# Performance work log

Hardware: AMD Instinct MI355X
Metric: run time of the kernel (lower is better)

The kernel has to match this reference:

```python
import jax, jax.numpy as jnp
import numpy as np

B, T, C, H = 65536, 100, 7, 2  # batch, timesteps, covariates, lstm hidden


def setup_inputs() -> dict:
    key = jax.random.key(0)
    ks = iter(jax.random.split(key, 32))
    def rn(shape, s=0.1):
        return jax.random.normal(next(ks), shape, dtype=jnp.float32) * s
    inp = {"x": jax.random.normal(next(ks), (B, T, C), dtype=jnp.float32)}
    for l, din in ((0, C), (1, 2 * H)):
        for suf in ("", "r"):
            inp[f"w_ih_l{l}{suf}"] = rn((4 * H, din))
            inp[f"w_hh_l{l}{suf}"] = rn((4 * H, H))
            inp[f"b_ih_l{l}{suf}"] = rn((4 * H,))
            inp[f"b_hh_l{l}{suf}"] = rn((4 * H,))
    inp["fc1_w"] = rn((64, 4 * T))
    inp["fc1_b"] = rn((64,))
    inp["fc2_w"] = rn((20, 64))
    inp["fc2_b"] = rn((20,))
    return inp


def _lstm_dir(xw, w_hh, b_hh, reverse):
    # xw: [T, B, 4H] precomputed input projection (x @ W_ih.T + b_ih)
    if reverse:
        xw = xw[::-1]
    h0 = jnp.zeros((xw.shape[1], H), xw.dtype)
    c0 = jnp.zeros((xw.shape[1], H), xw.dtype)

    def step(carry, gx):
        h, c = carry
        g = gx + h @ w_hh.T + b_hh            # [B, 4H]
        i, f, gg, o = jnp.split(g, 4, axis=-1)  # torch gate order i,f,g,o
        c = jax.nn.sigmoid(f) * c + jax.nn.sigmoid(i) * jnp.tanh(gg)
        h = jax.nn.sigmoid(o) * jnp.tanh(c)
        return (h, c), h

    _, hs = jax.lax.scan(step, (h0, c0), xw)
    if reverse:
        hs = hs[::-1]
    return hs  # [T, B, H]


def _bilstm_layer(x_tbf, w_ih_f, w_hh_f, b_ih_f, b_hh_f,
                  w_ih_b, w_hh_b, b_ih_b, b_hh_b):
    xw_f = jnp.einsum('tbc,gc->tbg', x_tbf, w_ih_f) + b_ih_f
    xw_b = jnp.einsum('tbc,gc->tbg', x_tbf, w_ih_b) + b_ih_b
    hf = _lstm_dir(xw_f, w_hh_f, b_hh_f, False)
    hb = _lstm_dir(xw_b, w_hh_b, b_hh_b, True)
    return jnp.concatenate([hf, hb], axis=-1)  # [T, B, 2H]


def reference(x,
              w_ih_l0, w_hh_l0, b_ih_l0, b_hh_l0,
              w_ih_l0r, w_hh_l0r, b_ih_l0r, b_hh_l0r,
              w_ih_l1, w_hh_l1, b_ih_l1, b_hh_l1,
              w_ih_l1r, w_hh_l1r, b_ih_l1r, b_hh_l1r,
              fc1_w, fc1_b, fc2_w, fc2_b):
    xt = jnp.transpose(x.reshape(-1, T, C), (1, 0, 2))  # [T, B, C] time-major
    h1 = _bilstm_layer(xt, w_ih_l0, w_hh_l0, b_ih_l0, b_hh_l0,
                       w_ih_l0r, w_hh_l0r, b_ih_l0r, b_hh_l0r)
    h2 = _bilstm_layer(h1, w_ih_l1, w_hh_l1, b_ih_l1, b_hh_l1,
                       w_ih_l1r, w_hh_l1r, b_ih_l1r, b_hh_l1r)
    out = jnp.transpose(h2, (1, 0, 2)).reshape(-1, 4 * T)  # flatten [B, 4T]
    out = jax.nn.relu(out)                  # relu BEFORE fc1, as in original
    out = jax.nn.relu(out @ fc1_w.T + fc1_b)
    return out @ fc2_w.T + fc2_b            # [B, 20]
```

## Files before the change

kernel.cpp:

```cpp
#include <hip/hip_runtime.h>

#define Bn 65536
#define Tn 100
#define Cn 7

typedef short short8 __attribute__((ext_vector_type(8)));
typedef float float4v __attribute__((ext_vector_type(4)));

__device__ __forceinline__ float fast_rcp(float x) { return __builtin_amdgcn_rcpf(x); }
__device__ __forceinline__ float sig_f(float x) { return fast_rcp(1.f + __expf(-x)); }
__device__ __forceinline__ float tanh_f(float x) { return 1.f - 2.f * fast_rcp(__expf(2.f * x) + 1.f); }
__device__ __forceinline__ unsigned bf16rne(float x) {
    unsigned u = __float_as_uint(x);
    return (u + 0x7fffu + ((u >> 16) & 1u)) >> 16;
}
__device__ __forceinline__ float bf_lo(unsigned u) { return __uint_as_float(u << 16); }
__device__ __forceinline__ float bf_hi(unsigned u) { return __uint_as_float(u & 0xffff0000u); }

typedef const __attribute__((address_space(1))) void* gp_t;
typedef __attribute__((address_space(3))) void* sp_t;
__device__ __forceinline__ void async_copy_dw(const void* g, void* l) {
    __builtin_amdgcn_global_load_lds((gp_t)g, (sp_t)l, 4, 0, 0);
}

__global__ void w2prep_kernel(const float* __restrict__ fc1_w, unsigned short* __restrict__ w2g) {
    int idx = blockIdx.x * 256 + threadIdx.x;
    int w  = idx >> 12;
    int d  = (idx >> 11) & 1;
    int n  = (idx >> 5) & 63;
    int kk = idx & 31;
    int tt = kk >> 1, i = kk & 1;
    int t  = d ? (99 - 10 * w - tt) : (10 * w + tt);
    float v = (kk < 20) ? fc1_w[n * 400 + 4 * t + 2 * d + i] : 0.f;
    w2g[idx] = (unsigned short)bf16rne(v);
}

__global__ __launch_bounds__(256) void l0_kernel(
    const float* __restrict__ x,
    const float* __restrict__ wih_f, const float* __restrict__ whh_f,
    const float* __restrict__ bih_f, const float* __restrict__ bhh_f,
    const float* __restrict__ wih_r, const float* __restrict__ whh_r,
    const float* __restrict__ bih_r, const float* __restrict__ bhh_r,
    unsigned* __restrict__ h1u)
{
    __shared__ float xs[2][2][4480];

    const int tid  = threadIdx.x;
    const int rev  = tid >> 7;
    const int s    = tid & 127;
    const int b    = blockIdx.x * 128 + s;
    const int w    = tid >> 6;
    const int lane = tid & 63;
    const int sdir = w >> 1;
    const int half = w & 1;

    const float* wih = rev ? wih_r : wih_f;
    const float* whh = rev ? whh_r : whh_f;
    const float* bih = rev ? bih_r : bih_f;
    const float* bhh = rev ? bhh_r : bhh_f;

    float wi[56], wh[16], bias[8];
#pragma unroll
    for (int k = 0; k < 56; ++k) wi[k] = wih[k];
#pragma unroll
    for (int k = 0; k < 16; ++k) wh[k] = whh[k];
#pragma unroll
    for (int k = 0; k < 8; ++k) bias[k] = bih[k] + bhh[k];

    const int e  = (lane >= 35) ? 1 : 0;
    const int r0 = lane - 35 * e;
    const int s0 = half * 64 + e;
    const float* xsamp = x + (size_t)(blockIdx.x * 128 + s0) * 700;

    auto stage = [&](int ch, int p) {
        const int off = sdir ? (665 - 35 * ch) : (35 * ch);
        const float* g = xsamp + off + r0;
        float* l = &xs[p][sdir][half * 2240 + lane];
        int r = r0;
#pragma unroll
        for (int i = 0; i < 35; ++i) {
            async_copy_dw(g, l);
            l += 64;
            const int c = (r >= 6) ? 1 : 0;
            g += c ? 1394 : 729;
            r += c ? -6 : 29;
        }
    };

    float h0 = 0.f, h1v = 0.f, c0 = 0.f, c1 = 0.f;

    stage(0, 0);
#pragma unroll 1
    for (int ch = 0; ch < 20; ++ch) {
        if (ch == 0) __builtin_amdgcn_s_waitcnt(0x0F70);
        else         __builtin_amdgcn_s_waitcnt(0x0F75);
        __syncthreads();
        if (ch < 19) stage(ch + 1, (ch + 1) & 1);
        __builtin_amdgcn_sched_barrier(0);

        const int t0 = rev ? (95 - 5 * ch) : (5 * ch);
        const float* xbuf = &xs[ch & 1][rev][0];
#pragma unroll
        for (int tt = 0; tt < 5; ++tt) {
            const int rr = rev ? (4 - tt) : tt;
            const int t  = t0 + rr;
            const float* xrow = xbuf + s * 35 + rr * 7;

            float g[8];
#pragma unroll
            for (int k = 0; k < 8; ++k) g[k] = bias[k];
#pragma unroll
            for (int c = 0; c < 7; ++c) {
                const float xv = xrow[c];
#pragma unroll
                for (int k = 0; k < 8; ++k) g[k] = fmaf(wi[k * 7 + c], xv, g[k]);
            }
#pragma unroll
            for (int k = 0; k < 8; ++k)
                g[k] = fmaf(wh[k * 2], h0, fmaf(wh[k * 2 + 1], h1v, g[k]));

            const float i0 = sig_f(g[0]), i1 = sig_f(g[1]);
            const float f0 = sig_f(g[2]), f1 = sig_f(g[3]);
            const float q0 = tanh_f(g[4]), q1 = tanh_f(g[5]);
            const float o0 = sig_f(g[6]), o1 = sig_f(g[7]);
            c0 = fmaf(f0, c0, i0 * q0);
            c1 = fmaf(f1, c1, i1 * q1);
            h0  = o0 * tanh_f(c0);
            h1v = o1 * tanh_f(c1);

            h1u[((size_t)t * 2 + rev) * Bn + b] = bf16rne(h0) | (bf16rne(h1v) << 16);
        }
    }
}

__global__ __launch_bounds__(256) void l1fc_kernel(
    const unsigned* __restrict__ hin,
    const float* __restrict__ wih_f, const float* __restrict__ whh_f,
    const float* __restrict__ bih_f, const float* __restrict__ bhh_f,
    const float* __restrict__ wih_r, const float* __restrict__ whh_r,
    const float* __restrict__ bih_r, const float* __restrict__ bhh_r,
    const unsigned* __restrict__ w2g,
    const float* __restrict__ fc1_b,
    const float* __restrict__ fc2_w,
    const float* __restrict__ fc2_b,
    float* __restrict__ out)
{
    __shared__ unsigned smem[19456];
    unsigned* a2  = smem;
    unsigned* w2b = smem + 5120;
    unsigned* hst = smem + 9216;

    const int tid  = threadIdx.x;
    const int ww   = tid >> 6;
    const int lane = tid & 63;
    const int d    = ww >> 1;
    const int half = ww & 1;
    const int sm   = half * 64 + lane;
    const int b0   = blockIdx.x * 128;

    const float* wih = d ? wih_r : wih_f;
    const float* whh = d ? whh_r : whh_f;
    const float* bih = d ? bih_r : bih_f;
    const float* bhh = d ? bhh_r : bhh_f;

    float wi[32], wh[16], bias[8];
#pragma unroll
    for (int k = 0; k < 32; ++k) wi[k] = wih[k];
#pragma unroll
    for (int k = 0; k < 16; ++k) wh[k] = whh[k];
#pragma unroll
    for (int k = 0; k < 8; ++k) bias[k] = bih[k] + bhh[k];

    float4v acc[2][4];
#pragma unroll
    for (int mt = 0; mt < 2; ++mt)
#pragma unroll
        for (int nt = 0; nt < 4; ++nt) acc[mt][nt] = (float4v){0.f, 0.f, 0.f, 0.f};

    for (int i = tid; i < 5120; i += 256) a2[i] = 0u;

    auto stage_h = [&](int w, int pb) {
        unsigned* dst = hst + pb * 5120;
        const int Rb = tid >> 7;
        const int s  = tid & 127;
#pragma unroll
        for (int i = 0; i < 20; ++i) {
            const int R  = Rb + 2 * i;
            const int dd = (R >= 20) ? 1 : 0;
            const int r2 = R - 20 * dd;
            const int p  = (r2 >= 10) ? 1 : 0;
            const int j  = r2 - 10 * p;
            const int t  = dd ? (99 - (10 * w + j)) : (10 * w + j);
            async_copy_dw(hin + ((size_t)t * 2 + p) * Bn + b0 + s, dst + R * 128 + s);
        }
    };
    auto stage_w = [&](int w, int pb) {
        const unsigned* src = w2g + w * 2048;
        unsigned* dst = w2b + pb * 2048;
#pragma unroll
        for (int i = 0; i < 8; ++i)
            async_copy_dw(src + i * 256 + tid, dst + i * 256 + tid);
    };

    stage_h(0, 0); stage_w(0, 0);

    float h0 = 0.f, h1v = 0.f, c0 = 0.f, c1 = 0.f;
    const int q = lane >> 4, l16 = lane & 15;

#pragma unroll 1
    for (int w = 0; w < 10; ++w) {
        __builtin_amdgcn_s_waitcnt(0x0F70);
        __syncthreads();
        if (w < 9) { stage_h(w + 1, (w + 1) & 1); stage_w(w + 1, (w + 1) & 1); }

        const unsigned* hb = hst + (w & 1) * 5120 + d * 2560;
#pragma unroll 2
        for (int j = 0; j < 10; ++j) {
            const unsigned uF = hb[j * 128 + sm];
            const unsigned uR = hb[1280 + j * 128 + sm];
            const float aF0 = bf_lo(uF), aF1 = bf_hi(uF);
            const float aR0 = bf_lo(uR), aR1 = bf_hi(uR);

            float g[8];
#pragma unroll
            for (int k = 0; k < 8; ++k) {
                g[k] = bias[k];
                g[k] = fmaf(wi[k * 4 + 0], aF0, g[k]);
                g[k] = fmaf(wi[k * 4 + 1], aF1, g[k]);
                g[k] = fmaf(wi[k * 4 + 2], aR0, g[k]);
                g[k] = fmaf(wi[k * 4 + 3], aR1, g[k]);
                g[k] = fmaf(wh[k * 2], h0, fmaf(wh[k * 2 + 1], h1v, g[k]));
            }
            const float i0 = sig_f(g[0]), i1 = sig_f(g[1]);
            const float f0 = sig_f(g[2]), f1 = sig_f(g[3]);
            const float q0 = tanh_f(g[4]), q1 = tanh_f(g[5]);
            const float o0 = sig_f(g[6]), o1 = sig_f(g[7]);
            c0 = fmaf(f0, c0, i0 * q0);
            c1 = fmaf(f1, c1, i1 * q1);
            h0  = o0 * tanh_f(c0);
            h1v = o1 * tanh_f(c1);

            a2[d * 2560 + sm * 20 + j] = bf16rne(fmaxf(h0, 0.f)) | (bf16rne(fmaxf(h1v, 0.f)) << 16);
        }
        __syncthreads();

        {
            const unsigned* wb = w2b + (w & 1) * 2048;
#pragma unroll
            for (int dd = 0; dd < 2; ++dd) {
                short8 av[2], bv[4];
#pragma unroll
                for (int mt = 0; mt < 2; ++mt)
                    av[mt] = *(const short8*)&a2[dd * 2560 + (ww * 32 + mt * 16 + l16) * 20 + q * 4];
#pragma unroll
                for (int nt = 0; nt < 4; ++nt)
                    bv[nt] = *(const short8*)&wb[dd * 1024 + (nt * 16 + l16) * 16 + q * 4];
#pragma unroll
                for (int mt = 0; mt < 2; ++mt)
#pragma unroll
                    for (int nt = 0; nt < 4; ++nt)
                        acc[mt][nt] = __builtin_amdgcn_mfma_f32_16x16x32_bf16(
                            av[mt], bv[nt], acc[mt][nt], 0, 0, 0);
            }
        }
    }
    __syncthreads();

    {
        float* eb = (float*)smem;
#pragma unroll
        for (int mt = 0; mt < 2; ++mt)
#pragma unroll
            for (int nt = 0; nt < 4; ++nt)
#pragma unroll
                for (int r = 0; r < 4; ++r) {
                    const int sl = ww * 32 + mt * 16 + q * 4 + r;
                    const int cl = nt * 16 + l16;
                    eb[sl * 65 + cl] = acc[mt][nt][r];
                }
    }
    __syncthreads();

    const float* eb = (const float*)smem;
    const int sm2 = tid & 127;
    const int og  = (tid >> 7) * 10;
    float z[64];
#pragma unroll
    for (int k = 0; k < 64; ++k) z[k] = fmaxf(eb[sm2 * 65 + k] + fc1_b[k], 0.f);
    float y[10];
#pragma unroll
    for (int o = 0; o < 10; ++o) {
        float r2 = fc2_b[og + o];
#pragma unroll
        for (int k = 0; k < 64; ++k) r2 = fmaf(fc2_w[(og + o) * 64 + k], z[k], r2);
        y[o] = r2;
    }
    __syncthreads();
    float* ebw = (float*)smem;
#pragma unroll
    for (int o = 0; o < 10; ++o) ebw[sm2 * 20 + og + o] = y[o];
    __syncthreads();
    for (int f = tid; f < 2560; f += 256)
        out[(size_t)blockIdx.x * 2560 + f] = ebw[f];
}

extern "C" void kernel_launch(void* const* d_in, const int* in_sizes, int n_in,
                              void* d_out, int out_size, void* d_ws, size_t ws_size,
                              hipStream_t stream) {
    const float* x = (const float*)d_in[0];
    const float* w_ih_l0  = (const float*)d_in[1];
    const float* w_hh_l0  = (const float*)d_in[2];
    const float* b_ih_l0  = (const float*)d_in[3];
    const float* b_hh_l0  = (const float*)d_in[4];
    const float* w_ih_l0r = (const float*)d_in[5];
    const float* w_hh_l0r = (const float*)d_in[6];
    const float* b_ih_l0r = (const float*)d_in[7];
    const float* b_hh_l0r = (const float*)d_in[8];
    const float* w_ih_l1  = (const float*)d_in[9];
    const float* w_hh_l1  = (const float*)d_in[10];
    const float* b_ih_l1  = (const float*)d_in[11];
    const float* b_hh_l1  = (const float*)d_in[12];
    const float* w_ih_l1r = (const float*)d_in[13];
    const float* w_hh_l1r = (const float*)d_in[14];
    const float* b_ih_l1r = (const float*)d_in[15];
    const float* b_hh_l1r = (const float*)d_in[16];
    const float* fc1_w = (const float*)d_in[17];
    const float* fc1_b = (const float*)d_in[18];
    const float* fc2_w = (const float*)d_in[19];
    const float* fc2_b = (const float*)d_in[20];

    unsigned* h1u = (unsigned*)d_ws;
    unsigned short* w2g = (unsigned short*)((char*)d_ws + (size_t)Tn * 2 * Bn * 4);

    w2prep_kernel<<<160, 256, 0, stream>>>(fc1_w, w2g);
    l0_kernel<<<512, 256, 0, stream>>>(x,
        w_ih_l0, w_hh_l0, b_ih_l0, b_hh_l0,
        w_ih_l0r, w_hh_l0r, b_ih_l0r, b_hh_l0r, h1u);
    l1fc_kernel<<<512, 256, 0, stream>>>(h1u,
        w_ih_l1, w_hh_l1, b_ih_l1, b_hh_l1,
        w_ih_l1r, w_hh_l1r, b_ih_l1r, b_hh_l1r,
        (const unsigned*)w2g, fc1_b, fc2_w, fc2_b, (float*)d_out);
}
```

Measured before the change: 433.5 us.

## Split LSTM hidden units across lane pairs with DPP exchange, double threads

```diff
diff --git a/kernel.cpp b/kernel.cpp
--- a/kernel.cpp
+++ b/kernel.cpp
@@ -16,6 +16,11 @@
 }
 __device__ __forceinline__ float bf_lo(unsigned u) { return __uint_as_float(u << 16); }
 __device__ __forceinline__ float bf_hi(unsigned u) { return __uint_as_float(u & 0xffff0000u); }
+
+__device__ __forceinline__ float dpp_xor1(float x) {
+    return __uint_as_float((unsigned)__builtin_amdgcn_mov_dpp(
+        (int)__float_as_uint(x), 0xB1, 0xF, 0xF, true));
+}
 
 typedef const __attribute__((address_space(1))) void* gp_t;
 typedef __attribute__((address_space(3))) void* sp_t;
@@ -35,7 +40,7 @@
     w2g[idx] = (unsigned short)bf16rne(v);
 }
 
-__global__ __launch_bounds__(256) void l0_kernel(
+__global__ __launch_bounds__(512) void l0_kernel(
     const float* __restrict__ x,
     const float* __restrict__ wih_f, const float* __restrict__ whh_f,
     const float* __restrict__ bih_f, const float* __restrict__ bhh_f,
@@ -46,36 +51,40 @@
     __shared__ float xs[2][2][4480];
 
     const int tid  = threadIdx.x;
-    const int rev  = tid >> 7;
-    const int s    = tid & 127;
+    const int wv   = tid >> 6;
+    const int lane = tid & 63;
+    const int rev  = tid >> 8;
+    const int cid  = tid & 1;
+    const int s    = (tid & 255) >> 1;
     const int b    = blockIdx.x * 128 + s;
-    const int w    = tid >> 6;
-    const int lane = tid & 63;
-    const int sdir = w >> 1;
-    const int half = w & 1;
 
     const float* wih = rev ? wih_r : wih_f;
     const float* whh = rev ? whh_r : whh_f;
     const float* bih = rev ? bih_r : bih_f;
     const float* bhh = rev ? bhh_r : bhh_f;
 
-    float wi[56], wh[16], bias[8];
-#pragma unroll
-    for (int k = 0; k < 56; ++k) wi[k] = wih[k];
-#pragma unroll
-    for (int k = 0; k < 16; ++k) wh[k] = whh[k];
-#pragma unroll
-    for (int k = 0; k < 8; ++k) bias[k] = bih[k] + bhh[k];
-
+    float wi[28], whA[4], whB[4], bias4[4];
+#pragma unroll
+    for (int j = 0; j < 4; ++j) {
+        const int k = cid + 2 * j;
+#pragma unroll
+        for (int c = 0; c < 7; ++c) wi[j * 7 + c] = wih[k * 7 + c];
+        whA[j] = whh[k * 2 + cid];
+        whB[j] = whh[k * 2 + (cid ^ 1)];
+        bias4[j] = bih[k] + bhh[k];
+    }
+
+    const int sdir  = (wv >> 1) & 1;
+    const int shalf = wv & 1;
     const int e  = (lane >= 35) ? 1 : 0;
     const int r0 = lane - 35 * e;
-    const int s0 = half * 64 + e;
+    const int s0 = shalf * 64 + e;
     const float* xsamp = x + (size_t)(blockIdx.x * 128 + s0) * 700;
 
     auto stage = [&](int ch, int p) {
         const int off = sdir ? (665 - 35 * ch) : (35 * ch);
         const float* g = xsamp + off + r0;
-        float* l = &xs[p][sdir][half * 2240 + lane];
+        float* l = &xs[p][sdir][shalf * 2240 + lane];
         int r = r0;
 #pragma unroll
         for (int i = 0; i < 35; ++i) {
@@ -87,53 +96,53 @@
         }
     };
 
-    float h0 = 0.f, h1v = 0.f, c0 = 0.f, c1 = 0.f;
-
-    stage(0, 0);
+    float hs = 0.f, ho = 0.f, cc = 0.f;
+
+    if (wv < 4) stage(0, 0);
 #pragma unroll 1
-    for (int ch = 0; ch < 20; ++ch) {
-        if (ch == 0) __builtin_amdgcn_s_waitcnt(0x0F70);
-        else         __builtin_amdgcn_s_waitcnt(0x0F75);
+    for (int chk = 0; chk < 20; ++chk) {
+        if (chk == 0) __builtin_amdgcn_s_waitcnt(0x0F70);
+        else          __builtin_amdgcn_s_waitcnt(0x0F75);
         __syncthreads();
-        if (ch < 19) stage(ch + 1, (ch + 1) & 1);
+        if (wv < 4 && chk < 19) stage(chk + 1, (chk + 1) & 1);
         __builtin_amdgcn_sched_barrier(0);
 
-        const int t0 = rev ? (95 - 5 * ch) : (5 * ch);
-        const float* xbuf = &xs[ch & 1][rev][0];
+        const int t0 = rev ? (95 - 5 * chk) : (5 * chk);
+        const float* xbuf = &xs[chk & 1][rev][0];
 #pragma unroll
         for (int tt = 0; tt < 5; ++tt) {
             const int rr = rev ? (4 - tt) : tt;
             const int t  = t0 + rr;
             const float* xrow = xbuf + s * 35 + rr * 7;
 
-            float g[8];
-#pragma unroll
-            for (int k = 0; k < 8; ++k) g[k] = bias[k];
+            float g[4];
+#pragma unroll
+            for (int j = 0; j < 4; ++j) g[j] = bias4[j];
 #pragma unroll
             for (int c = 0; c < 7; ++c) {
                 const float xv = xrow[c];
 #pragma unroll
-                for (int k = 0; k < 8; ++k) g[k] = fmaf(wi[k * 7 + c], xv, g[k]);
+                for (int j = 0; j < 4; ++j) g[j] = fmaf(wi[j * 7 + c], xv, g[j]);
             }
 #pragma unroll
-            for (int k = 0; k < 8; ++k)
-                g[k] = fmaf(wh[k * 2], h0, fmaf(wh[k * 2 + 1], h1v, g[k]));
-
-            const float i0 = sig_f(g[0]), i1 = sig_f(g[1]);
-            const float f0 = sig_f(g[2]), f1 = sig_f(g[3]);
-            const float q0 = tanh_f(g[4]), q1 = tanh_f(g[5]);
-            const float o0 = sig_f(g[6]), o1 = sig_f(g[7]);
-            c0 = fmaf(f0, c0, i0 * q0);
-            c1 = fmaf(f1, c1, i1 * q1);
-            h0  = o0 * tanh_f(c0);
-            h1v = o1 * tanh_f(c1);
-
-            h1u[((size_t)t * 2 + rev) * Bn + b] = bf16rne(h0) | (bf16rne(h1v) << 16);
-        }
-    }
-}
-
-__global__ __launch_bounds__(256) void l1fc_kernel(
+            for (int j = 0; j < 4; ++j)
+                g[j] = fmaf(whA[j], hs, fmaf(whB[j], ho, g[j]));
+
+            const float iv = sig_f(g[0]);
+            const float fv = sig_f(g[1]);
+            const float qv = tanh_f(g[2]);
+            const float ov = sig_f(g[3]);
+            cc = fmaf(fv, cc, iv * qv);
+            hs = ov * tanh_f(cc);
+            ho = dpp_xor1(hs);
+
+            if (cid == 0)
+                h1u[((size_t)t * 2 + rev) * Bn + b] = bf16rne(hs) | (bf16rne(ho) << 16);
+        }
+    }
+}
+
+__global__ __launch_bounds__(512) void l1fc_kernel(
     const unsigned* __restrict__ hin,
     const float* __restrict__ wih_f, const float* __restrict__ whh_f,
     const float* __restrict__ bih_f, const float* __restrict__ bhh_f,
@@ -151,11 +160,11 @@
     unsigned* hst = smem + 9216;
 
     const int tid  = threadIdx.x;
-    const int ww   = tid >> 6;
+    const int wv   = tid >> 6;
     const int lane = tid & 63;
-    const int d    = ww >> 1;
-    const int half = ww & 1;
-    const int sm   = half * 64 + lane;
+    const int d    = tid >> 8;
+    const int cid  = tid & 1;
+    const int s    = (tid & 255) >> 1;
     const int b0   = blockIdx.x * 128;
 
     const float* wih = d ? wih_r : wih_f;
@@ -163,48 +172,49 @@
     const float* bih = d ? bih_r : bih_f;
     const float* bhh = d ? bhh_r : bhh_f;
 
-    float wi[32], wh[16], bias[8];
-#pragma unroll
-    for (int k = 0; k < 32; ++k) wi[k] = wih[k];
-#pragma unroll
-    for (int k = 0; k < 16; ++k) wh[k] = whh[k];
-#pragma unroll
-    for (int k = 0; k < 8; ++k) bias[k] = bih[k] + bhh[k];
-
-    float4v acc[2][4];
-#pragma unroll
-    for (int mt = 0; mt < 2; ++mt)
-#pragma unroll
-        for (int nt = 0; nt < 4; ++nt) acc[mt][nt] = (float4v){0.f, 0.f, 0.f, 0.f};
-
-    for (int i = tid; i < 5120; i += 256) a2[i] = 0u;
+    float wi[16], whA[4], whB[4], bias4[4];
+#pragma unroll
+    for (int j = 0; j < 4; ++j) {
+        const int k = cid + 2 * j;
+#pragma unroll
+        for (int m = 0; m < 4; ++m) wi[j * 4 + m] = wih[k * 4 + m];
+        whA[j] = whh[k * 2 + cid];
+        whB[j] = whh[k * 2 + (cid ^ 1)];
+        bias4[j] = bih[k] + bhh[k];
+    }
+
+    float4v acc[4];
+#pragma unroll
+    for (int nt = 0; nt < 4; ++nt) acc[nt] = (float4v){0.f, 0.f, 0.f, 0.f};
+
+    for (int i = tid; i < 5120; i += 512) a2[i] = 0u;
 
     auto stage_h = [&](int w, int pb) {
         unsigned* dst = hst + pb * 5120;
         const int Rb = tid >> 7;
-        const int s  = tid & 127;
-#pragma unroll
-        for (int i = 0; i < 20; ++i) {
-            const int R  = Rb + 2 * i;
+        const int s2 = tid & 127;
+#pragma unroll
+        for (int i = 0; i < 10; ++i) {
+            const int R  = Rb + 4 * i;
             const int dd = (R >= 20) ? 1 : 0;
             const int r2 = R - 20 * dd;
             const int p  = (r2 >= 10) ? 1 : 0;
             const int j  = r2 - 10 * p;
             const int t  = dd ? (99 - (10 * w + j)) : (10 * w + j);
-            async_copy_dw(hin + ((size_t)t * 2 + p) * Bn + b0 + s, dst + R * 128 + s);
+            async_copy_dw(hin + ((size_t)t * 2 + p) * Bn + b0 + s2, dst + R * 128 + s2);
         }
     };
     auto stage_w = [&](int w, int pb) {
         const unsigned* src = w2g + w * 2048;
         unsigned* dst = w2b + pb * 2048;
 #pragma unroll
-        for (int i = 0; i < 8; ++i)
-            async_copy_dw(src + i * 256 + tid, dst + i * 256 + tid);
+        for (int i = 0; i < 4; ++i)
+            async_copy_dw(src + i * 512 + tid, dst + i * 512 + tid);
     };
 
     stage_h(0, 0); stage_w(0, 0);
 
-    float h0 = 0.f, h1v = 0.f, c0 = 0.f, c1 = 0.f;
+    float hs = 0.f, ho = 0.f, cc = 0.f;
     const int q = lane >> 4, l16 = lane & 15;
 
 #pragma unroll 1
@@ -216,31 +226,32 @@
         const unsigned* hb = hst + (w & 1) * 5120 + d * 2560;
 #pragma unroll 2
         for (int j = 0; j < 10; ++j) {
-            const unsigned uF = hb[j * 128 + sm];
-            const unsigned uR = hb[1280 + j * 128 + sm];
+            const unsigned uF = hb[j * 128 + s];
+            const unsigned uR = hb[1280 + j * 128 + s];
             const float aF0 = bf_lo(uF), aF1 = bf_hi(uF);
             const float aR0 = bf_lo(uR), aR1 = bf_hi(uR);
 
-            float g[8];
-#pragma unroll
-            for (int k = 0; k < 8; ++k) {
-                g[k] = bias[k];
-                g[k] = fmaf(wi[k * 4 + 0], aF0, g[k]);
-                g[k] = fmaf(wi[k * 4 + 1], aF1, g[k]);
-                g[k] = fmaf(wi[k * 4 + 2], aR0, g[k]);
-                g[k] = fmaf(wi[k * 4 + 3], aR1, g[k]);
-                g[k] = fmaf(wh[k * 2], h0, fmaf(wh[k * 2 + 1], h1v, g[k]));
+            float g[4];
+#pragma unroll
+            for (int jj = 0; jj < 4; ++jj) {
+                g[jj] = bias4[jj];
+                g[jj] = fmaf(wi[jj * 4 + 0], aF0, g[jj]);
+                g[jj] = fmaf(wi[jj * 4 + 1], aF1, g[jj]);
+                g[jj] = fmaf(wi[jj * 4 + 2], aR0, g[jj]);
+                g[jj] = fmaf(wi[jj * 4 + 3], aR1, g[jj]);
+                g[jj] = fmaf(whA[jj], hs, fmaf(whB[jj], ho, g[jj]));
             }
-            const float i0 = sig_f(g[0]), i1 = sig_f(g[1]);
-            const float f0 = sig_f(g[2]), f1 = sig_f(g[3]);
-            const float q0 = tanh_f(g[4]), q1 = tanh_f(g[5]);
-            const float o0 = sig_f(g[6]), o1 = sig_f(g[7]);
-            c0 = fmaf(f0, c0, i0 * q0);
-            c1 = fmaf(f1, c1, i1 * q1);
-            h0  = o0 * tanh_f(c0);
-            h1v = o1 * tanh_f(c1);
-
-            a2[d * 2560 + sm * 20 + j] = bf16rne(fmaxf(h0, 0.f)) | (bf16rne(fmaxf(h1v, 0.f)) << 16);
+            const float iv = sig_f(g[0]);
+            const float fv = sig_f(g[1]);
+            const float qv = tanh_f(g[2]);
+            const float ov = sig_f(g[3]);
+            cc = fmaf(fv, cc, iv * qv);
+            hs = ov * tanh_f(cc);
+            ho = dpp_xor1(hs);
+
+            if (cid == 0)
+                a2[d * 2560 + s * 20 + j] =
+                    bf16rne(fmaxf(hs, 0.f)) | (bf16rne(fmaxf(ho, 0.f)) << 16);
         }
         __syncthreads();
 
@@ -248,19 +259,15 @@
             const unsigned* wb = w2b + (w & 1) * 2048;
 #pragma unroll
             for (int dd = 0; dd < 2; ++dd) {
-                short8 av[2], bv[4];
-#pragma unroll
-                for (int mt = 0; mt < 2; ++mt)
-                    av[mt] = *(const short8*)&a2[dd * 2560 + (ww * 32 + mt * 16 + l16) * 20 + q * 4];
+                short8 av = *(const short8*)&a2[dd * 2560 + (wv * 16 + l16) * 20 + q * 4];
+                short8 bv[4];
 #pragma unroll
                 for (int nt = 0; nt < 4; ++nt)
                     bv[nt] = *(const short8*)&wb[dd * 1024 + (nt * 16 + l16) * 16 + q * 4];
 #pragma unroll
-                for (int mt = 0; mt < 2; ++mt)
-#pragma unroll
-                    for (int nt = 0; nt < 4; ++nt)
-                        acc[mt][nt] = __builtin_amdgcn_mfma_f32_16x16x32_bf16(
-                            av[mt], bv[nt], acc[mt][nt], 0, 0, 0);
+                for (int nt = 0; nt < 4; ++nt)
+                    acc[nt] = __builtin_amdgcn_mfma_f32_16x16x32_bf16(
+                        av, bv[nt], acc[nt], 0, 0, 0);
             }
         }
     }
@@ -269,27 +276,25 @@
     {
         float* eb = (float*)smem;
 #pragma unroll
-        for (int mt = 0; mt < 2; ++mt)
-#pragma unroll
-            for (int nt = 0; nt < 4; ++nt)
-#pragma unroll
-                for (int r = 0; r < 4; ++r) {
-                    const int sl = ww * 32 + mt * 16 + q * 4 + r;
-                    const int cl = nt * 16 + l16;
-                    eb[sl * 65 + cl] = acc[mt][nt][r];
-                }
+        for (int nt = 0; nt < 4; ++nt)
+#pragma unroll
+            for (int r = 0; r < 4; ++r) {
+                const int sl = wv * 16 + q * 4 + r;
+                const int cl = nt * 16 + l16;
+                eb[sl * 65 + cl] = acc[nt][r];
+            }
     }
     __syncthreads();
 
     const float* eb = (const float*)smem;
     const int sm2 = tid & 127;
-    const int og  = (tid >> 7) * 10;
+    const int og  = (tid >> 7) * 5;
     float z[64];
 #pragma unroll
     for (int k = 0; k < 64; ++k) z[k] = fmaxf(eb[sm2 * 65 + k] + fc1_b[k], 0.f);
-    float y[10];
-#pragma unroll
-    for (int o = 0; o < 10; ++o) {
+    float y[5];
+#pragma unroll
+    for (int o = 0; o < 5; ++o) {
         float r2 = fc2_b[og + o];
 #pragma unroll
         for (int k = 0; k < 64; ++k) r2 = fmaf(fc2_w[(og + o) * 64 + k], z[k], r2);
@@ -298,9 +303,9 @@
     __syncthreads();
     float* ebw = (float*)smem;
 #pragma unroll
-    for (int o = 0; o < 10; ++o) ebw[sm2 * 20 + og + o] = y[o];
+    for (int o = 0; o < 5; ++o) ebw[sm2 * 20 + og + o] = y[o];
     __syncthreads();
-    for (int f = tid; f < 2560; f += 256)
+    for (int f = tid; f < 2560; f += 512)
         out[(size_t)blockIdx.x * 2560 + f] = ebw[f];
 }
 
@@ -333,10 +338,10 @@
     unsigned short* w2g = (unsigned short*)((char*)d_ws + (size_t)Tn * 2 * Bn * 4);
 
     w2prep_kernel<<<160, 256, 0, stream>>>(fc1_w, w2g);
-    l0_kernel<<<512, 256, 0, stream>>>(x,
+    l0_kernel<<<512, 512, 0, stream>>>(x,
         w_ih_l0, w_hh_l0, b_ih_l0, b_hh_l0,
         w_ih_l0r, w_hh_l0r, b_ih_l0r, b_hh_l0r, h1u);
-    l1fc_kernel<<<512, 256, 0, stream>>>(h1u,
+    l1fc_kernel<<<512, 512, 0, stream>>>(h1u,
         w_ih_l1, w_hh_l1, b_ih_l1, b_hh_l1,
         w_ih_l1r, w_hh_l1r, b_ih_l1r, b_hh_l1r,
         (const unsigned*)w2g, fc1_b, fc2_w, fc2_b, (float*)d_out);
```

New measurement: 430.6 us. No clear change (-0.7%).
